# Performance work log

Hardware: AMD Instinct MI355X
Metric: run time of the kernel (lower is better)

The kernel has to match this reference:

```python
import jax, jax.numpy as jnp
import numpy as np

N = 50000      # nodes
E = 640000     # edges
D = 128        # in_dims == hidden_dims == out_dims (heads=1)
PE_DIM = 37
NTYPES = 9     # n_edge_types + 1
L = 3          # n_layers


def setup_inputs() -> dict:
    key = jax.random.key(0)
    ks = jax.random.split(key, 16)
    s = 0.1
    return {
        "X_n": jax.random.normal(ks[0], (N, D), jnp.float32),
        "PE": jax.random.normal(ks[1], (N, PE_DIM), jnp.float32),
        "edge_index": jax.random.randint(ks[2], (2, E), 0, N, jnp.int32),
        "edge_attr": jax.random.randint(ks[3], (E,), 0, NTYPES, jnp.int32),
        # stacked per-layer parameters (all layers share dims since heads=1)
        "edge_emb": jax.random.normal(ks[4], (L, NTYPES, D), jnp.float32) * s,
        "pe_W": jax.random.normal(ks[5], (L, PE_DIM, D), jnp.float32) * s,   # pe MLP modeled as single Linear
        "pe_b": jnp.zeros((L, D), jnp.float32),
        "lin_W": jax.random.normal(ks[6], (L, D, D), jnp.float32) * s,      # [in,out] layout: h @ W
        "attn_l": jax.random.normal(ks[7], (L, D), jnp.float32) * s,
        "attn_r": jax.random.normal(ks[8], (L, D), jnp.float32) * s,
        "attn_e": jax.random.normal(ks[9], (L, D), jnp.float32) * s,
        "bias": jnp.zeros((L, D), jnp.float32),
        "bn_gamma": jnp.ones((L - 1, D), jnp.float32),
        "bn_beta": jnp.zeros((L - 1, D), jnp.float32),
    }


def _gat_forward(X_n, PE, edge_emb, pe_W, pe_b, lin_W, attn_l, attn_r,
                 attn_e, bias, bn_gamma, bn_beta, src, dst, edge_attr):
    x = X_n
    for l in range(L):
        x0 = x
        # PE embedding + linear projection (heads=1 -> per-head dim = D)
        h = x + PE @ pe_W[l] + pe_b[l]
        h = h @ lin_W[l]                                  # [N, D]
        # per-edge attention logits
        xe_score = (edge_emb[l][edge_attr] * attn_e[l]).sum(-1)   # [E]
        hj = h[src]                                       # gather source feats [E, D]
        alpha = hj @ attn_l[l] + (h @ attn_r[l])[dst] + xe_score  # [E]
        alpha = jnp.where(alpha > 0, alpha, 0.2 * alpha)  # leaky_relu(0.2)
        # scatter-softmax over incoming edges of each target node
        amax = jax.ops.segment_max(alpha, dst, num_segments=N)
        e = jnp.exp(alpha - amax[dst])
        denom = jax.ops.segment_sum(e, dst, num_segments=N)
        a = e / denom[dst]                                # [E]
        # weighted scatter-add aggregation
        out = jax.ops.segment_sum(a[:, None] * hj, dst, num_segments=N) + bias[l]
        if l < L - 1:
            # BatchNorm1d in training mode (batch statistics, biased var)
            mu = out.mean(0)
            var = ((out - mu) ** 2).mean(0)
            out = (out - mu) / jnp.sqrt(var + 1e-5) * bn_gamma[l] + bn_beta[l]
        x = out + x0                                      # residual
    return x


def reference(X_n, edge_index, edge_attr, PE, edge_emb, pe_W, pe_b, lin_W,
              attn_l, attn_r, attn_e, bias, bn_gamma, bn_beta):
    src, dst = edge_index[0], edge_index[1]
    return _gat_forward(X_n, PE, edge_emb, pe_W, pe_b, lin_W, attn_l, attn_r,
                        attn_e, bias, bn_gamma, bn_beta, src, dst, edge_attr)
```

## Files before the change

kernel.cpp:

```cpp
#include <hip/hip_runtime.h>
#include <hip/hip_bf16.h>
#include <math.h>

#define NNODES 50000
#define NEDGES 640000
#define DIM    128
#define PEDIM  37
#define KTOT   165
#define KPAD   200
#define PEPAD  64
#define HSTR   136
#define NLAYERS 3
#define NSB    ((NNODES + 255) / 256)
#define NPEB   ((NNODES * 8 + 255) / 256)
#define NGSC   16

using bf16x8 = __attribute__((ext_vector_type(8))) short;
using f32x4  = __attribute__((ext_vector_type(4))) float;

static constexpr size_t alignup(size_t x) { return (x + 255) & ~size_t(255); }
static constexpr size_t OFF_X1   = 0;
static constexpr size_t OFF_X2   = alignup(OFF_X1  + (size_t)NNODES * DIM * 4);
static constexpr size_t OFF_O    = alignup(OFF_X2  + (size_t)NNODES * DIM * 4);
static constexpr size_t OFF_H    = alignup(OFF_O   + (size_t)NNODES * DIM * 4);
static constexpr size_t OFF_PEB  = alignup(OFF_H   + (size_t)NNODES * DIM * 2);
static constexpr size_t OFF_HL   = alignup(OFF_PEB + (size_t)NNODES * PEPAD * 2);
static constexpr size_t OFF_HR   = alignup(OFF_HL  + (size_t)NNODES * 4);
static constexpr size_t OFF_OFFS = alignup(OFF_HR  + (size_t)NNODES * 4);
static constexpr size_t OFF_CUR  = alignup(OFF_OFFS + (size_t)(NNODES + 1) * 4);
static constexpr size_t OFF_CSR  = alignup(OFF_CUR + (size_t)NNODES * 4);
static constexpr size_t OFF_BTG  = alignup(OFF_CSR + (size_t)NEDGES * 4);
static constexpr size_t OFF_B2   = alignup(OFF_BTG + 3 * (size_t)DIM * KPAD * 2);
static constexpr size_t OFF_ET   = alignup(OFF_B2  + 3 * DIM * 4);
static constexpr size_t OFF_GS   = alignup(OFF_ET  + 3 * 16 * 4);
static constexpr size_t OFF_BS   = alignup(OFF_GS  + 2 * NGSC * 256 * 4);
static constexpr size_t OFF_BP   = alignup(OFF_BS  + 256 * 4);
static constexpr size_t WS_NEED  = alignup(OFF_BP  + 256 * 4);

__device__ inline unsigned short f2b(float f) {
    union { float f; unsigned int u; } x; x.f = f;
    unsigned int r = x.u + 0x7FFFu + ((x.u >> 16) & 1u);
    return (unsigned short)(r >> 16);
}
__device__ inline unsigned int pack2(float a, float b) {
    return (unsigned int)f2b(a) | ((unsigned int)f2b(b) << 16);
}

__device__ inline void gload_lds16(const void* g, void* l) {
    __builtin_amdgcn_global_load_lds((const __attribute__((address_space(1))) void*)g,
                                     (__attribute__((address_space(3))) void*)l, 16, 0, 0);
}


__global__ void k_zero_int(int* __restrict__ p, int n) {
    for (int i = blockIdx.x * blockDim.x + threadIdx.x; i < n; i += gridDim.x * blockDim.x)
        p[i] = 0;
}

__global__ void k_count(const int* __restrict__ dstv, int* __restrict__ cnt) {
    for (int e = blockIdx.x * blockDim.x + threadIdx.x; e < NEDGES; e += gridDim.x * blockDim.x)
        atomicAdd(&cnt[dstv[e]], 1);
}

__global__ __launch_bounds__(256) void k_scan1(const int* __restrict__ cnt, int* __restrict__ bsum) {
    __shared__ int ls[256];
    const int i = blockIdx.x * 256 + threadIdx.x;
    ls[threadIdx.x] = (i < NNODES) ? cnt[i] : 0;
    __syncthreads();
    for (int d = 128; d > 0; d >>= 1) {
        if (threadIdx.x < d) ls[threadIdx.x] += ls[threadIdx.x + d];
        __syncthreads();
    }
    if (threadIdx.x == 0) bsum[blockIdx.x] = ls[0];
}

__global__ __launch_bounds__(256) void k_scan2(const int* __restrict__ bsum,
                                               int* __restrict__ bpre, int* __restrict__ offs) {
    __shared__ int ls[256];
    const int t = threadIdx.x;
    ls[t] = (t < NSB) ? bsum[t] : 0;
    __syncthreads();
    for (int d = 1; d < 256; d <<= 1) {
        int v = (t >= d) ? ls[t - d] : 0;
        __syncthreads();
        ls[t] += v;
        __syncthreads();
    }
    bpre[t] = (t == 0) ? 0 : ls[t - 1];
    if (t == 255) offs[NNODES] = ls[255];
}

__global__ __launch_bounds__(256) void k_scan3(const int* __restrict__ cnt,
                                               const int* __restrict__ bpre,
                                               int* __restrict__ offs, int* __restrict__ cur) {
    __shared__ int ls[256];
    const int i = blockIdx.x * 256 + threadIdx.x;
    const int v = (i < NNODES) ? cnt[i] : 0;
    ls[threadIdx.x] = v;
    __syncthreads();
    for (int d = 1; d < 256; d <<= 1) {
        int x = (threadIdx.x >= d) ? ls[threadIdx.x - d] : 0;
        __syncthreads();
        ls[threadIdx.x] += x;
        __syncthreads();
    }
    if (i < NNODES) {
        const int excl = ls[threadIdx.x] - v + bpre[blockIdx.x];
        offs[i] = excl;
        cur[i] = excl;
    }
}

__global__ void k_fill(const int* __restrict__ srcv, const int* __restrict__ dstv,
                       const int* __restrict__ attr, int* __restrict__ cur,
                       int* __restrict__ csr) {
    for (int e = blockIdx.x * blockDim.x + threadIdx.x; e < NEDGES; e += gridDim.x * blockDim.x) {
        int d = dstv[e];
        int pos = atomicAdd(&cur[d], 1);
        csr[pos] = (srcv[e] & 0xFFFF) | (attr[e] << 16);
    }
}

__device__ inline void params_body(int pb, int tid,
    const float* __restrict__ linW, const float* __restrict__ peW,
    const float* __restrict__ peb, const float* __restrict__ attn_e,
    const float* __restrict__ edge_emb,
    unsigned short* __restrict__ Btg, float* __restrict__ b2, float* __restrict__ et) {
    if (pb < 100) {
        const int idx = pb * 256 + tid;
        const int j = idx & 127;
        const int k = idx >> 7;
        float v = 0.f;
        if (k < DIM) {
            v = linW[k * DIM + j];
        } else if (k < KTOT) {
            const int p = k - DIM;
            float s = 0.f;
            #pragma unroll 8
            for (int d = 0; d < DIM; ++d) s = fmaf(peW[p * DIM + d], linW[d * DIM + j], s);
            v = s;
        }
        Btg[(size_t)j * KPAD + k] = f2b(v);
    } else {
        if (tid < DIM) {
            float s = 0.f;
            #pragma unroll 8
            for (int d = 0; d < DIM; ++d) s = fmaf(peb[d], linW[d * DIM + tid], s);
            b2[tid] = s;
        } else if (tid < DIM + 9) {
            const int e = tid - DIM;
            float s = 0.f;
            #pragma unroll 8
            for (int d = 0; d < DIM; ++d) s = fmaf(edge_emb[e * DIM + d], attn_e[d], s);
            et[e] = s;
        }
    }
}

__global__ __launch_bounds__(256) void k_pack(
    const float* __restrict__ PE,
    const float* __restrict__ lin_W, const float* __restrict__ pe_W,
    const float* __restrict__ pe_b, const float* __restrict__ attn_e,
    const float* __restrict__ edge_emb,
    unsigned short* __restrict__ PEb, unsigned short* __restrict__ Btg,
    float* __restrict__ b2, float* __restrict__ et, float* __restrict__ gs) {
    const int b = blockIdx.x;
    if (b < NPEB) {
        const int idx = b * 256 + threadIdx.x;
        if (idx >= NNODES * 8) return;
        const int r = idx >> 3, q = idx & 7;
        float f[8];
        #pragma unroll
        for (int i = 0; i < 8; ++i) {
            const int ci = q * 8 + i;
            f[i] = (ci < PEDIM) ? PE[(size_t)r * PEDIM + ci] : 0.f;
        }
        int4 pk;
        pk.x = pack2(f[0], f[1]); pk.y = pack2(f[2], f[3]);
        pk.z = pack2(f[4], f[5]); pk.w = pack2(f[6], f[7]);
        ((int4*)(PEb + (size_t)r * PEPAD))[q] = pk;
    } else if (b < NPEB + 3 * 101) {
        const int pidx = b - NPEB;
        const int l = pidx / 101, pb = pidx % 101;
        params_body(pb, threadIdx.x,
                    lin_W + (size_t)l * DIM * DIM, pe_W + (size_t)l * PEDIM * DIM,
                    pe_b + (size_t)l * DIM, attn_e + (size_t)l * DIM,
                    edge_emb + (size_t)l * 9 * DIM,
                    Btg + (size_t)l * DIM * KPAD, b2 + l * DIM, et + l * 16);
    } else {
        for (int i = threadIdx.x; i < 2 * NGSC * 256; i += 256) gs[i] = 0.f;
    }
}

template<int L0>
__global__ __launch_bounds__(256) void k_gemm(
    const void* __restrict__ OPREV, const float* __restrict__ XPREV,
    const float* __restrict__ gsrc, const float* __restrict__ gamma,
    const float* __restrict__ beta, float* __restrict__ XNEXT,
    const unsigned short* __restrict__ PEb, const unsigned short* __restrict__ Btg,
    const float* __restrict__ b2, const float* __restrict__ attn_l,
    const float* __restrict__ attn_r,
    unsigned short* __restrict__ H, float* __restrict__ HL, float* __restrict__ HR) {
    __shared__ unsigned short Bls[DIM * KPAD];
    __shared__ float smu[DIM], ssc[DIM], sbt[DIM];
    const int tid = threadIdx.x;
    const int row0 = blockIdx.x * 64;
    const int w = tid >> 6, l = tid & 63;
    const int c = l & 15;
    const int g = l >> 4;
    const int row = row0 + w * 16 + c;
    const bool ok = row < NNODES;

    float4 oxf[4][2], xpv[4][2];
    int4 oxb[4];
    #pragma unroll
    for (int s = 0; s < 4; ++s) {
        const int col0 = g * 8 + s * 32;
        const float4 z = {0.f, 0.f, 0.f, 0.f};
        xpv[s][0] = z; xpv[s][1] = z;
        if (L0) {
            oxf[s][0] = z; oxf[s][1] = z;
            if (ok) {
                const float4* op = (const float4*)&((const float*)OPREV)[((size_t)row << 7) + col0];
                oxf[s][0] = op[0]; oxf[s][1] = op[1];
            }
        } else {
            oxb[s] = make_int4(0, 0, 0, 0);
            if (ok) {
                oxb[s] = *(const int4*)&((const unsigned short*)OPREV)[((size_t)row << 7) + col0];
                const float4* xp = (const float4*)&XPREV[((size_t)row << 7) + col0];
                xpv[s][0] = xp[0]; xpv[s][1] = xp[1];
            }
        }
    }
    int4 pe4 = {0, 0, 0, 0}, pe5 = {0, 0, 0, 0};
    if (ok) {
        const int4* pp = (const int4*)(PEb + (size_t)row * PEPAD);
        pe4 = pp[g];
        pe5 = pp[4 + g];
    }

    {
        const int4* gb = (const int4*)Btg;
        int4* lb = (int4*)Bls;
        for (int i = tid; i < 3200; i += 256) gload_lds16(gb + i, lb + i);
    }
    if (!L0 && tid < DIM) {
        float s = 0.f, s2 = 0.f;
        #pragma unroll
        for (int q = 0; q < NGSC; ++q) {
            s += gsrc[q * 256 + tid];
            s2 += gsrc[q * 256 + 128 + tid];
        }
        const float mu = s * (1.f / NNODES);
        const float var = s2 * (1.f / NNODES) - mu * mu;
        smu[tid] = mu;
        ssc[tid] = gamma[tid] * rsqrtf(var + 1e-5f);
        sbt[tid] = beta[tid];
    }
    __syncthreads();

    bf16x8 af[6];
    #pragma unroll
    for (int s = 0; s < 4; ++s) {
        const int col0 = g * 8 + s * 32;
        float xn[8];
        if (L0) {
            xn[0] = oxf[s][0].x; xn[1] = oxf[s][0].y; xn[2] = oxf[s][0].z; xn[3] = oxf[s][0].w;
            xn[4] = oxf[s][1].x; xn[5] = oxf[s][1].y; xn[6] = oxf[s][1].z; xn[7] = oxf[s][1].w;
        } else {
            const unsigned int u0 = (unsigned)oxb[s].x, u1 = (unsigned)oxb[s].y;
            const unsigned int u2 = (unsigned)oxb[s].z, u3 = (unsigned)oxb[s].w;
            float ov[8];
            ov[0] = __uint_as_float(u0 << 16); ov[1] = __uint_as_float(u0 & 0xFFFF0000u);
            ov[2] = __uint_as_float(u1 << 16); ov[3] = __uint_as_float(u1 & 0xFFFF0000u);
            ov[4] = __uint_as_float(u2 << 16); ov[5] = __uint_as_float(u2 & 0xFFFF0000u);
            ov[6] = __uint_as_float(u3 << 16); ov[7] = __uint_as_float(u3 & 0xFFFF0000u);
            const float4 mu0 = *(const float4*)&smu[col0], mu1 = *(const float4*)&smu[col0 + 4];
            const float4 sc0 = *(const float4*)&ssc[col0], sc1 = *(const float4*)&ssc[col0 + 4];
            const float4 bt0 = *(const float4*)&sbt[col0], bt1 = *(const float4*)&sbt[col0 + 4];
            xn[0] = (ov[0] - mu0.x) * sc0.x + bt0.x + xpv[s][0].x;
            xn[1] = (ov[1] - mu0.y) * sc0.y + bt0.y + xpv[s][0].y;
            xn[2] = (ov[2] - mu0.z) * sc0.z + bt0.z + xpv[s][0].z;
            xn[3] = (ov[3] - mu0.w) * sc0.w + bt0.w + xpv[s][0].w;
            xn[4] = (ov[4] - mu1.x) * sc1.x + bt1.x + xpv[s][1].x;
            xn[5] = (ov[5] - mu1.y) * sc1.y + bt1.y + xpv[s][1].y;
            xn[6] = (ov[6] - mu1.z) * sc1.z + bt1.z + xpv[s][1].z;
            xn[7] = (ov[7] - mu1.w) * sc1.w + bt1.w + xpv[s][1].w;
            if (ok) {
                float4* xo = (float4*)&XNEXT[((size_t)row << 7) + col0];
                xo[0] = make_float4(xn[0], xn[1], xn[2], xn[3]);
                xo[1] = make_float4(xn[4], xn[5], xn[6], xn[7]);
            }
        }
        int4 pk;
        pk.x = pack2(xn[0], xn[1]); pk.y = pack2(xn[2], xn[3]);
        pk.z = pack2(xn[4], xn[5]); pk.w = pack2(xn[6], xn[7]);
        af[s] = *(const bf16x8*)&pk;
    }
    af[4] = *(const bf16x8*)&pe4;
    af[5] = *(const bf16x8*)&pe5;

    f32x4 zero4 = {0.f, 0.f, 0.f, 0.f};
    f32x4 acc[8];
    #pragma unroll
    for (int t = 0; t < 8; ++t) acc[t] = zero4;

    #pragma unroll
    for (int t = 0; t < 8; ++t) {
        const unsigned short* bRow = Bls + (size_t)(t * 16 + c) * KPAD + g * 8;
        #pragma unroll
        for (int s = 0; s < 6; ++s)
            acc[t] = __builtin_amdgcn_mfma_f32_16x16x32_bf16(af[s], *(const bf16x8*)(bRow + s * 32), acc[t], 0, 0, 0);
    }

    float b2v[8], alv[8], arv[8];
    #pragma unroll
    for (int t = 0; t < 8; ++t) {
        b2v[t] = b2[t * 16 + c];
        alv[t] = attn_l[t * 16 + c];
        arv[t] = attn_r[t * 16 + c];
    }
    #pragma unroll
    for (int t = 0; t < 8; ++t)
        #pragma unroll
        for (int j = 0; j < 4; ++j) acc[t][j] += b2v[t];

    #pragma unroll
    for (int j = 0; j < 4; ++j) {
        float sl = 0.f, sr = 0.f;
        #pragma unroll
        for (int t = 0; t < 8; ++t) { sl = fmaf(acc[t][j], alv[t], sl); sr = fmaf(acc[t][j], arv[t], sr); }
        #pragma unroll
        for (int m = 1; m < 16; m <<= 1) {
            sl += __shfl_xor(sl, m, 64);
            sr += __shfl_xor(sr, m, 64);
        }
        const int grow = row0 + w * 16 + g * 4 + j;
        if (grow < NNODES && c == 0) { HL[grow] = sl; HR[grow] = sr; }
    }

    __syncthreads();
    unsigned short* Hls = Bls;
    #pragma unroll
    for (int t = 0; t < 8; ++t)
        #pragma unroll
        for (int j = 0; j < 4; ++j)
            Hls[(w * 16 + g * 4 + j) * HSTR + t * 16 + c] = f2b(acc[t][j]);
    __syncthreads();
    #pragma unroll
    for (int kb = 0; kb < 4; ++kb) {
        const int idx = tid + kb * 256;
        const int r = idx >> 4, kc = idx & 15;
        const int grow = row0 + r;
        if (grow < NNODES) {
            const int4 v = *(const int4*)(Hls + r * HSTR + kc * 8);
            ((int4*)(H + ((size_t)grow << 7)))[kc] = v;
        }
    }
}

template<int FINAL>
__global__ __launch_bounds__(256) void k_agg(
    const int* __restrict__ offs, const int* __restrict__ csr,
    const float* __restrict__ HL, const float* __restrict__ HR,
    const float* __restrict__ et, const unsigned short* __restrict__ H,
    const float* __restrict__ bias, const float* __restrict__ xprev,
    void* __restrict__ OUTv) {
    const int lane = threadIdx.x & 63;
    const int node = blockIdx.x * 4 + (threadIdx.x >> 6);
    const int off0 = offs[node];
    const int deg = offs[node + 1] - off0;

    const float hri = HR[node];
    float myA = 0.f;
    int myE = 0;
    float mx = -1e30f;
    for (int j = lane; j < deg; j += 64) {
        const int en = csr[off0 + j];
        float al = HL[en & 0xFFFF] + hri + et[en >> 16];
        al = al > 0.f ? al : 0.2f * al;
        if (j < 64) { myA = al; myE = en & 0xFFFF; }
        mx = fmaxf(mx, al);
    }
    #pragma unroll
    for (int m = 1; m < 64; m <<= 1) mx = fmaxf(mx, __shfl_xor(mx, m, 64));

    float s = 0.f, wv = 0.f;
    const bool small = deg <= 64;
    if (small) {
        wv = (lane < deg) ? __expf(myA - mx) : 0.f;
        s = wv;
    } else {
        for (int j = lane; j < deg; j += 64) {
            const int en = csr[off0 + j];
            float al = HL[en & 0xFFFF] + hri + et[en >> 16];
            al = al > 0.f ? al : 0.2f * al;
            s += __expf(al - mx);
        }
    }
    #pragma unroll
    for (int m = 1; m < 64; m <<= 1) s += __shfl_xor(s, m, 64);
    const float invd = (deg > 0) ? 1.f / s : 0.f;
    wv *= invd;

    const int eg = lane >> 4, c = lane & 15;
    float a[8];
    #pragma unroll
    for (int t = 0; t < 8; ++t) a[t] = 0.f;

    if (small) {
        for (int jb = 0; jb < deg; jb += 16) {
            float wl[4];
            int sl[4];
            #pragma unroll
            for (int u = 0; u < 4; ++u) {
                const int j = jb + eg + u * 4;
                wl[u] = __shfl(wv, j & 63, 64);
                sl[u] = __shfl(myE, j & 63, 64);
                if (j >= deg) wl[u] = 0.f;
            }
            int4 hv0 = *(const int4*)(H + ((size_t)sl[0] << 7) + (c << 3));
            int4 hv1 = *(const int4*)(H + ((size_t)sl[1] << 7) + (c << 3));
            int4 hv2 = *(const int4*)(H + ((size_t)sl[2] << 7) + (c << 3));
            int4 hv3 = *(const int4*)(H + ((size_t)sl[3] << 7) + (c << 3));
            const int4 hvv[4] = {hv0, hv1, hv2, hv3};
            #pragma unroll
            for (int u = 0; u < 4; ++u) {
                const unsigned int ux = (unsigned)hvv[u].x, uy = (unsigned)hvv[u].y;
                const unsigned int uz = (unsigned)hvv[u].z, uw = (unsigned)hvv[u].w;
                const float wg = wl[u];
                a[0] = fmaf(wg, __uint_as_float(ux << 16), a[0]);
                a[1] = fmaf(wg, __uint_as_float(ux & 0xFFFF0000u), a[1]);
                a[2] = fmaf(wg, __uint_as_float(uy << 16), a[2]);
                a[3] = fmaf(wg, __uint_as_float(uy & 0xFFFF0000u), a[3]);
                a[4] = fmaf(wg, __uint_as_float(uz << 16), a[4]);
                a[5] = fmaf(wg, __uint_as_float(uz & 0xFFFF0000u), a[5]);
                a[6] = fmaf(wg, __uint_as_float(uw << 16), a[6]);
                a[7] = fmaf(wg, __uint_as_float(uw & 0xFFFF0000u), a[7]);
            }
        }
    } else {
        for (int jb = 0; jb < deg; jb += 8) {
            float wl[2];
            int sl[2];
            #pragma unroll
            for (int u = 0; u < 2; ++u) {
                const int j = jb + eg + u * 4;
                wl[u] = 0.f; sl[u] = 0;
                if (j < deg) {
                    const int en = csr[off0 + j];
                    sl[u] = en & 0xFFFF;
                    float al = HL[sl[u]] + hri + et[en >> 16];
                    al = al > 0.f ? al : 0.2f * al;
                    wl[u] = __expf(al - mx) * invd;
                }
            }
            int4 hv0 = *(const int4*)(H + ((size_t)sl[0] << 7) + (c << 3));
            int4 hv1 = *(const int4*)(H + ((size_t)sl[1] << 7) + (c << 3));
            const int4 hvv[2] = {hv0, hv1};
            #pragma unroll
            for (int u = 0; u < 2; ++u) {
                const unsigned int ux = (unsigned)hvv[u].x, uy = (unsigned)hvv[u].y;
                const unsigned int uz = (unsigned)hvv[u].z, uw = (unsigned)hvv[u].w;
                const float wg = wl[u];
                a[0] = fmaf(wg, __uint_as_float(ux << 16), a[0]);
                a[1] = fmaf(wg, __uint_as_float(ux & 0xFFFF0000u), a[1]);
                a[2] = fmaf(wg, __uint_as_float(uy << 16), a[2]);
                a[3] = fmaf(wg, __uint_as_float(uy & 0xFFFF0000u), a[3]);
                a[4] = fmaf(wg, __uint_as_float(uz << 16), a[4]);
                a[5] = fmaf(wg, __uint_as_float(uz & 0xFFFF0000u), a[5]);
                a[6] = fmaf(wg, __uint_as_float(uw << 16), a[6]);
                a[7] = fmaf(wg, __uint_as_float(uw & 0xFFFF0000u), a[7]);
            }
        }
    }

    #pragma unroll
    for (int m = 16; m < 64; m <<= 1)
        #pragma unroll
        for (int t = 0; t < 8; ++t) a[t] += __shfl_xor(a[t], m, 64);

    if (eg == 0) {
        float o[8];
        const float* bp = bias + (c << 3);
        #pragma unroll
        for (int t = 0; t < 8; ++t) o[t] = a[t] + bp[t];
        if (FINAL) {
            float* OUT = (float*)OUTv;
            const float* xp = xprev + ((size_t)node << 7) + (c << 3);
            #pragma unroll
            for (int t = 0; t < 8; ++t) o[t] += xp[t];
            float* op = OUT + ((size_t)node << 7) + (c << 3);
            *(float4*)(op)     = make_float4(o[0], o[1], o[2], o[3]);
            *(float4*)(op + 4) = make_float4(o[4], o[5], o[6], o[7]);
        } else {
            unsigned short* OUT = (unsigned short*)OUTv;
            int4 pk;
            pk.x = pack2(o[0], o[1]); pk.y = pack2(o[2], o[3]);
            pk.z = pack2(o[4], o[5]); pk.w = pack2(o[6], o[7]);
            *(int4*)(OUT + ((size_t)node << 7) + (c << 3)) = pk;
        }
    }
}

__global__ __launch_bounds__(256) void k_bnstats(
    const unsigned short* __restrict__ OUT, float* __restrict__ gs) {
    __shared__ float lsl[256], lsh[256], l2l[256], l2h[256];
    const int c2 = threadIdx.x & 63;
    const int q  = threadIdx.x >> 6;
    const int rend = min(NNODES, (int)(blockIdx.x * 256 + 256));
    const unsigned int* U = (const unsigned int*)OUT;
    float sl = 0.f, sh = 0.f, s2l = 0.f, s2h = 0.f;
    for (int r = blockIdx.x * 256 + q; r < rend; r += 4) {
        const unsigned int u = U[(size_t)r * 64 + c2];
        const float lo = __uint_as_float(u << 16);
        const float hi = __uint_as_float(u & 0xFFFF0000u);
        sl += lo; sh += hi;
        s2l = fmaf(lo, lo, s2l); s2h = fmaf(hi, hi, s2h);
    }
    lsl[threadIdx.x] = sl; lsh[threadIdx.x] = sh;
    l2l[threadIdx.x] = s2l; l2h[threadIdx.x] = s2h;
    __syncthreads();
    if (threadIdx.x < 64) {
        float a0 = 0.f, a1 = 0.f, a2 = 0.f, a3 = 0.f;
        #pragma unroll
        for (int k = 0; k < 4; ++k) {
            a0 += lsl[k * 64 + c2]; a1 += lsh[k * 64 + c2];
            a2 += l2l[k * 64 + c2]; a3 += l2h[k * 64 + c2];
        }
        const int qq = blockIdx.x & (NGSC - 1);
        atomicAdd(&gs[qq * 256 + 2 * c2], a0);
        atomicAdd(&gs[qq * 256 + 2 * c2 + 1], a1);
        atomicAdd(&gs[qq * 256 + 128 + 2 * c2], a2);
        atomicAdd(&gs[qq * 256 + 128 + 2 * c2 + 1], a3);
    }
}

extern "C" void kernel_launch(void* const* d_in, const int* in_sizes, int n_in,
                              void* d_out, int out_size, void* d_ws, size_t ws_size,
                              hipStream_t stream) {
    const float* X_n      = (const float*)d_in[0];
    const float* PE       = (const float*)d_in[1];
    const int*   eidx     = (const int*)d_in[2];
    const int*   eattr    = (const int*)d_in[3];
    const float* edge_emb = (const float*)d_in[4];
    const float* pe_W     = (const float*)d_in[5];
    const float* pe_b     = (const float*)d_in[6];
    const float* lin_W    = (const float*)d_in[7];
    const float* attn_l   = (const float*)d_in[8];
    const float* attn_r   = (const float*)d_in[9];
    const float* attn_e   = (const float*)d_in[10];
    const float* bias     = (const float*)d_in[11];
    const float* bng      = (const float*)d_in[12];
    const float* bnb      = (const float*)d_in[13];

    if (ws_size < WS_NEED) return;

    char* ws = (char*)d_ws;
    float* x1     = (float*)(ws + OFF_X1);
    float* x2     = (float*)(ws + OFF_X2);
    unsigned short* obufb = (unsigned short*)(ws + OFF_O);
    unsigned short* hbuf  = (unsigned short*)(ws + OFF_H);
    unsigned short* PEb   = (unsigned short*)(ws + OFF_PEB);
    float* hl     = (float*)(ws + OFF_HL);
    float* hr     = (float*)(ws + OFF_HR);
    int*   offs   = (int*)(ws + OFF_OFFS);
    int*   cur    = (int*)(ws + OFF_CUR);
    int*   csr    = (int*)(ws + OFF_CSR);
    unsigned short* Btg = (unsigned short*)(ws + OFF_BTG);
    float* b2     = (float*)(ws + OFF_B2);
    float* et     = (float*)(ws + OFF_ET);
    float* gs     = (float*)(ws + OFF_GS);
    int*   bsum   = (int*)(ws + OFF_BS);
    int*   bpre   = (int*)(ws + OFF_BP);

    const int* srcv = eidx;
    const int* dstv = eidx + NEDGES;

    hipLaunchKernelGGL(k_zero_int, dim3(256), dim3(256), 0, stream, cur, NNODES);
    hipLaunchKernelGGL(k_count, dim3(1024), dim3(256), 0, stream, dstv, cur);
    hipLaunchKernelGGL(k_scan1, dim3(NSB), dim3(256), 0, stream, cur, bsum);
    hipLaunchKernelGGL(k_scan2, dim3(1), dim3(256), 0, stream, bsum, bpre, offs);
    hipLaunchKernelGGL(k_scan3, dim3(NSB), dim3(256), 0, stream, cur, bpre, offs, cur);
    hipLaunchKernelGGL(k_fill, dim3(1024), dim3(256), 0, stream, srcv, dstv, eattr, cur, csr);
    hipLaunchKernelGGL(k_pack, dim3(NPEB + 3 * 101 + 1), dim3(256), 0, stream,
                       PE, lin_W, pe_W, pe_b, attn_e, edge_emb, PEb, Btg, b2, et, gs);

    const int NGB = (NNODES + 63) / 64;
    hipLaunchKernelGGL((k_gemm<1>), dim3(NGB), dim3(256), 0, stream,
                       (const void*)X_n, (const float*)nullptr, (const float*)nullptr,
                       (const float*)nullptr, (const float*)nullptr, (float*)nullptr,
                       PEb, Btg, b2, attn_l, attn_r, hbuf, hl, hr);
    hipLaunchKernelGGL((k_agg<0>), dim3(NNODES / 4), dim3(256), 0, stream,
                       offs, csr, hl, hr, et, hbuf, bias, (const float*)nullptr, (void*)obufb);
    hipLaunchKernelGGL(k_bnstats, dim3(NSB), dim3(256), 0, stream, obufb, gs);
    hipLaunchKernelGGL((k_gemm<0>), dim3(NGB), dim3(256), 0, stream,
                       (const void*)obufb, X_n, gs, bng, bnb, x1,
                       PEb, Btg + (size_t)DIM * KPAD, b2 + DIM, attn_l + DIM, attn_r + DIM,
                       hbuf, hl, hr);
    hipLaunchKernelGGL((k_agg<0>), dim3(NNODES / 4), dim3(256), 0, stream,
                       offs, csr, hl, hr, et + 16, hbuf, bias + DIM, (const float*)nullptr, (void*)obufb);
    hipLaunchKernelGGL(k_bnstats, dim3(NSB), dim3(256), 0, stream, obufb, gs + NGSC * 256);
    hipLaunchKernelGGL((k_gemm<0>), dim3(NGB), dim3(256), 0, stream,
                       (const void*)obufb, x1, gs + NGSC * 256, bng + DIM, bnb + DIM, x2,
                       PEb, Btg + 2 * (size_t)DIM * KPAD, b2 + 2 * DIM, attn_l + 2 * DIM, attn_r + 2 * DIM,
                       hbuf, hl, hr);
    hipLaunchKernelGGL((k_agg<1>), dim3(NNODES / 4), dim3(256), 0, stream,
                       offs, csr, hl, hr, et + 32, hbuf, bias + 2 * DIM, x2,
                       (void*)d_out);
}
```

Before: 275.5 us.

## Bucket CSR fill in two passes and store residual activations as bf16

The CSR build now runs in two passes. Edges are first scattered into 32-node buckets using one atomic counter per bucket, padded to 64 bytes. A second per-bucket kernel then sorts each bucket by node in LDS and writes the result with coalesced stores. This is meant to cut global atomic contention and scattered writes, at the cost of an extra kernel and a temp buffer. Separately, the intermediate residual states x1/x2 are stored as bf16 instead of fp32, which halves their read/write traffic but adds rounding error to the residual path.

```diff
diff --git a/kernel.cpp b/kernel.cpp
--- a/kernel.cpp
+++ b/kernel.cpp
@@ -14,22 +14,26 @@
 #define NSB    ((NNODES + 255) / 256)
 #define NPEB   ((NNODES * 8 + 255) / 256)
 #define NGSC   16
+#define NBUCK  ((NNODES + 31) / 32)
+#define FCAP   1280
 
 using bf16x8 = __attribute__((ext_vector_type(8))) short;
 using f32x4  = __attribute__((ext_vector_type(4))) float;
 
 static constexpr size_t alignup(size_t x) { return (x + 255) & ~size_t(255); }
 static constexpr size_t OFF_X1   = 0;
-static constexpr size_t OFF_X2   = alignup(OFF_X1  + (size_t)NNODES * DIM * 4);
-static constexpr size_t OFF_O    = alignup(OFF_X2  + (size_t)NNODES * DIM * 4);
-static constexpr size_t OFF_H    = alignup(OFF_O   + (size_t)NNODES * DIM * 4);
+static constexpr size_t OFF_X2   = alignup(OFF_X1  + (size_t)NNODES * DIM * 2);
+static constexpr size_t OFF_O    = alignup(OFF_X2  + (size_t)NNODES * DIM * 2);
+static constexpr size_t OFF_H    = alignup(OFF_O   + (size_t)NNODES * DIM * 2);
 static constexpr size_t OFF_PEB  = alignup(OFF_H   + (size_t)NNODES * DIM * 2);
 static constexpr size_t OFF_HL   = alignup(OFF_PEB + (size_t)NNODES * PEPAD * 2);
 static constexpr size_t OFF_HR   = alignup(OFF_HL  + (size_t)NNODES * 4);
 static constexpr size_t OFF_OFFS = alignup(OFF_HR  + (size_t)NNODES * 4);
 static constexpr size_t OFF_CUR  = alignup(OFF_OFFS + (size_t)(NNODES + 1) * 4);
 static constexpr size_t OFF_CSR  = alignup(OFF_CUR + (size_t)NNODES * 4);
-static constexpr size_t OFF_BTG  = alignup(OFF_CSR + (size_t)NEDGES * 4);
+static constexpr size_t OFF_TMP  = alignup(OFF_CSR + (size_t)NEDGES * 4);
+static constexpr size_t OFF_BCUR = alignup(OFF_TMP + (size_t)NEDGES * 4);
+static constexpr size_t OFF_BTG  = alignup(OFF_BCUR + (size_t)NBUCK * 64);
 static constexpr size_t OFF_B2   = alignup(OFF_BTG + 3 * (size_t)DIM * KPAD * 2);
 static constexpr size_t OFF_ET   = alignup(OFF_B2  + 3 * DIM * 4);
 static constexpr size_t OFF_GS   = alignup(OFF_ET  + 3 * 16 * 4);
@@ -92,7 +96,8 @@
 
 __global__ __launch_bounds__(256) void k_scan3(const int* __restrict__ cnt,
                                                const int* __restrict__ bpre,
-                                               int* __restrict__ offs, int* __restrict__ cur) {
+                                               int* __restrict__ offs, int* __restrict__ cur,
+                                               int* __restrict__ bcur) {
     __shared__ int ls[256];
     const int i = blockIdx.x * 256 + threadIdx.x;
     const int v = (i < NNODES) ? cnt[i] : 0;
@@ -108,16 +113,52 @@
         const int excl = ls[threadIdx.x] - v + bpre[blockIdx.x];
         offs[i] = excl;
         cur[i] = excl;
-    }
-}
-
-__global__ void k_fill(const int* __restrict__ srcv, const int* __restrict__ dstv,
-                       const int* __restrict__ attr, int* __restrict__ cur,
-                       int* __restrict__ csr) {
+        if ((i & 31) == 0) bcur[(i >> 5) * 16] = excl;
+    }
+}
+
+__global__ void k_fillA(const int* __restrict__ srcv, const int* __restrict__ dstv,
+                        const int* __restrict__ attr, int* __restrict__ bcur,
+                        int* __restrict__ tmp) {
     for (int e = blockIdx.x * blockDim.x + threadIdx.x; e < NEDGES; e += gridDim.x * blockDim.x) {
-        int d = dstv[e];
-        int pos = atomicAdd(&cur[d], 1);
-        csr[pos] = (srcv[e] & 0xFFFF) | (attr[e] << 16);
+        const int d = dstv[e];
+        const int pos = atomicAdd(&bcur[(d >> 5) * 16], 1);
+        tmp[pos] = (srcv[e] & 0xFFFF) | (attr[e] << 16) | ((d & 31) << 20);
+    }
+}
+
+__global__ __launch_bounds__(256) void k_fillB(const int* __restrict__ offs,
+                                               const int* __restrict__ tmp,
+                                               int* __restrict__ cur, int* __restrict__ csr) {
+    __shared__ int cur32[32];
+    __shared__ int sdata[FCAP];
+    const int b = blockIdx.x;
+    const int nb = b * 32;
+    const int nbe = min(nb + 32, NNODES);
+    const int start = offs[nb];
+    const int end = offs[nbe];
+    const int size = end - start;
+    if (threadIdx.x < 32) {
+        const int node = nb + threadIdx.x;
+        cur32[threadIdx.x] = ((node < nbe) ? offs[node] : end) - start;
+    }
+    __syncthreads();
+    if (size <= FCAP) {
+        for (int i = threadIdx.x; i < size; i += 256) {
+            const int v = tmp[start + i];
+            const int p = atomicAdd(&cur32[(v >> 20) & 31], 1);
+            sdata[p] = v & 0xFFFFF;
+        }
+        __syncthreads();
+        for (int i = threadIdx.x; i < size; i += 256)
+            csr[start + i] = sdata[i];
+    } else {
+        for (int i = threadIdx.x; i < size; i += 256) {
+            const int v = tmp[start + i];
+            const int node = nb + ((v >> 20) & 31);
+            const int p = atomicAdd(&cur[node], 1);
+            csr[p] = v & 0xFFFFF;
+        }
     }
 }
 
@@ -192,11 +233,11 @@
     }
 }
 
-template<int L0>
+template<int MODE>
 __global__ __launch_bounds__(256) void k_gemm(
-    const void* __restrict__ OPREV, const float* __restrict__ XPREV,
+    const void* __restrict__ OPREV, const void* __restrict__ XPREV,
     const float* __restrict__ gsrc, const float* __restrict__ gamma,
-    const float* __restrict__ beta, float* __restrict__ XNEXT,
+    const float* __restrict__ beta, unsigned short* __restrict__ XNEXT,
     const unsigned short* __restrict__ PEb, const unsigned short* __restrict__ Btg,
     const float* __restrict__ b2, const float* __restrict__ attn_l,
     const float* __restrict__ attn_r,
@@ -211,14 +252,13 @@
     const int row = row0 + w * 16 + c;
     const bool ok = row < NNODES;
 
-    float4 oxf[4][2], xpv[4][2];
-    int4 oxb[4];
+    float4 oxf[4][2], xpf[4][2];
+    int4 oxb[4], xpb[4];
     #pragma unroll
     for (int s = 0; s < 4; ++s) {
         const int col0 = g * 8 + s * 32;
         const float4 z = {0.f, 0.f, 0.f, 0.f};
-        xpv[s][0] = z; xpv[s][1] = z;
-        if (L0) {
+        if (MODE == 0) {
             oxf[s][0] = z; oxf[s][1] = z;
             if (ok) {
                 const float4* op = (const float4*)&((const float*)OPREV)[((size_t)row << 7) + col0];
@@ -226,10 +266,16 @@
             }
         } else {
             oxb[s] = make_int4(0, 0, 0, 0);
-            if (ok) {
-                oxb[s] = *(const int4*)&((const unsigned short*)OPREV)[((size_t)row << 7) + col0];
-                const float4* xp = (const float4*)&XPREV[((size_t)row << 7) + col0];
-                xpv[s][0] = xp[0]; xpv[s][1] = xp[1];
+            if (ok) oxb[s] = *(const int4*)&((const unsigned short*)OPREV)[((size_t)row << 7) + col0];
+            if (MODE == 1) {
+                xpf[s][0] = z; xpf[s][1] = z;
+                if (ok) {
+                    const float4* xp = (const float4*)&((const float*)XPREV)[((size_t)row << 7) + col0];
+                    xpf[s][0] = xp[0]; xpf[s][1] = xp[1];
+                }
+            } else {
+                xpb[s] = make_int4(0, 0, 0, 0);
+                if (ok) xpb[s] = *(const int4*)&((const unsigned short*)XPREV)[((size_t)row << 7) + col0];
             }
         }
     }
@@ -245,7 +291,7 @@
         int4* lb = (int4*)Bls;
         for (int i = tid; i < 3200; i += 256) gload_lds16(gb + i, lb + i);
     }
-    if (!L0 && tid < DIM) {
+    if (MODE != 0 && tid < DIM) {
         float s = 0.f, s2 = 0.f;
         #pragma unroll
         for (int q = 0; q < NGSC; ++q) {
@@ -265,7 +311,7 @@
     for (int s = 0; s < 4; ++s) {
         const int col0 = g * 8 + s * 32;
         float xn[8];
-        if (L0) {
+        if (MODE == 0) {
             xn[0] = oxf[s][0].x; xn[1] = oxf[s][0].y; xn[2] = oxf[s][0].z; xn[3] = oxf[s][0].w;
             xn[4] = oxf[s][1].x; xn[5] = oxf[s][1].y; xn[6] = oxf[s][1].z; xn[7] = oxf[s][1].w;
         } else {
@@ -276,26 +322,35 @@
             ov[2] = __uint_as_float(u1 << 16); ov[3] = __uint_as_float(u1 & 0xFFFF0000u);
             ov[4] = __uint_as_float(u2 << 16); ov[5] = __uint_as_float(u2 & 0xFFFF0000u);
             ov[6] = __uint_as_float(u3 << 16); ov[7] = __uint_as_float(u3 & 0xFFFF0000u);
+            float xv[8];
+            if (MODE == 1) {
+                xv[0] = xpf[s][0].x; xv[1] = xpf[s][0].y; xv[2] = xpf[s][0].z; xv[3] = xpf[s][0].w;
+                xv[4] = xpf[s][1].x; xv[5] = xpf[s][1].y; xv[6] = xpf[s][1].z; xv[7] = xpf[s][1].w;
+            } else {
+                const unsigned int p0 = (unsigned)xpb[s].x, p1 = (unsigned)xpb[s].y;
+                const unsigned int p2 = (unsigned)xpb[s].z, p3 = (unsigned)xpb[s].w;
+                xv[0] = __uint_as_float(p0 << 16); xv[1] = __uint_as_float(p0 & 0xFFFF0000u);
+                xv[2] = __uint_as_float(p1 << 16); xv[3] = __uint_as_float(p1 & 0xFFFF0000u);
+                xv[4] = __uint_as_float(p2 << 16); xv[5] = __uint_as_float(p2 & 0xFFFF0000u);
+                xv[6] = __uint_as_float(p3 << 16); xv[7] = __uint_as_float(p3 & 0xFFFF0000u);
+            }
             const float4 mu0 = *(const float4*)&smu[col0], mu1 = *(const float4*)&smu[col0 + 4];
             const float4 sc0 = *(const float4*)&ssc[col0], sc1 = *(const float4*)&ssc[col0 + 4];
             const float4 bt0 = *(const float4*)&sbt[col0], bt1 = *(const float4*)&sbt[col0 + 4];
-            xn[0] = (ov[0] - mu0.x) * sc0.x + bt0.x + xpv[s][0].x;
-            xn[1] = (ov[1] - mu0.y) * sc0.y + bt0.y + xpv[s][0].y;
-            xn[2] = (ov[2] - mu0.z) * sc0.z + bt0.z + xpv[s][0].z;
-            xn[3] = (ov[3] - mu0.w) * sc0.w + bt0.w + xpv[s][0].w;
-            xn[4] = (ov[4] - mu1.x) * sc1.x + bt1.x + xpv[s][1].x;
-            xn[5] = (ov[5] - mu1.y) * sc1.y + bt1.y + xpv[s][1].y;
-            xn[6] = (ov[6] - mu1.z) * sc1.z + bt1.z + xpv[s][1].z;
-            xn[7] = (ov[7] - mu1.w) * sc1.w + bt1.w + xpv[s][1].w;
-            if (ok) {
-                float4* xo = (float4*)&XNEXT[((size_t)row << 7) + col0];
-                xo[0] = make_float4(xn[0], xn[1], xn[2], xn[3]);
-                xo[1] = make_float4(xn[4], xn[5], xn[6], xn[7]);
-            }
+            xn[0] = (ov[0] - mu0.x) * sc0.x + bt0.x + xv[0];
+            xn[1] = (ov[1] - mu0.y) * sc0.y + bt0.y + xv[1];
+            xn[2] = (ov[2] - mu0.z) * sc0.z + bt0.z + xv[2];
+            xn[3] = (ov[3] - mu0.w) * sc0.w + bt0.w + xv[3];
+            xn[4] = (ov[4] - mu1.x) * sc1.x + bt1.x + xv[4];
+            xn[5] = (ov[5] - mu1.y) * sc1.y + bt1.y + xv[5];
+            xn[6] = (ov[6] - mu1.z) * sc1.z + bt1.z + xv[6];
+            xn[7] = (ov[7] - mu1.w) * sc1.w + bt1.w + xv[7];
         }
         int4 pk;
         pk.x = pack2(xn[0], xn[1]); pk.y = pack2(xn[2], xn[3]);
         pk.z = pack2(xn[4], xn[5]); pk.w = pack2(xn[6], xn[7]);
+        if (MODE != 0 && ok)
+            *(int4*)&XNEXT[((size_t)row << 7) + col0] = pk;
         af[s] = *(const bf16x8*)&pk;
     }
     af[4] = *(const bf16x8*)&pe4;
@@ -365,7 +420,7 @@
     const int* __restrict__ offs, const int* __restrict__ csr,
     const float* __restrict__ HL, const float* __restrict__ HR,
     const float* __restrict__ et, const unsigned short* __restrict__ H,
-    const float* __restrict__ bias, const float* __restrict__ xprev,
+    const float* __restrict__ bias, const unsigned short* __restrict__ xprev,
     void* __restrict__ OUTv) {
     const int lane = threadIdx.x & 63;
     const int node = blockIdx.x * 4 + (threadIdx.x >> 6);
@@ -488,9 +543,13 @@
         for (int t = 0; t < 8; ++t) o[t] = a[t] + bp[t];
         if (FINAL) {
             float* OUT = (float*)OUTv;
-            const float* xp = xprev + ((size_t)node << 7) + (c << 3);
-            #pragma unroll
-            for (int t = 0; t < 8; ++t) o[t] += xp[t];
+            const int4 xb = *(const int4*)(xprev + ((size_t)node << 7) + (c << 3));
+            const unsigned int p0 = (unsigned)xb.x, p1 = (unsigned)xb.y;
+            const unsigned int p2 = (unsigned)xb.z, p3 = (unsigned)xb.w;
+            o[0] += __uint_as_float(p0 << 16); o[1] += __uint_as_float(p0 & 0xFFFF0000u);
+            o[2] += __uint_as_float(p1 << 16); o[3] += __uint_as_float(p1 & 0xFFFF0000u);
+            o[4] += __uint_as_float(p2 << 16); o[5] += __uint_as_float(p2 & 0xFFFF0000u);
+            o[6] += __uint_as_float(p3 << 16); o[7] += __uint_as_float(p3 & 0xFFFF0000u);
             float* op = OUT + ((size_t)node << 7) + (c << 3);
             *(float4*)(op)     = make_float4(o[0], o[1], o[2], o[3]);
             *(float4*)(op + 4) = make_float4(o[4], o[5], o[6], o[7]);
@@ -558,8 +617,8 @@
     if (ws_size < WS_NEED) return;
 
     char* ws = (char*)d_ws;
-    float* x1     = (float*)(ws + OFF_X1);
-    float* x2     = (float*)(ws + OFF_X2);
+    unsigned short* x1    = (unsigned short*)(ws + OFF_X1);
+    unsigned short* x2    = (unsigned short*)(ws + OFF_X2);
     unsigned short* obufb = (unsigned short*)(ws + OFF_O);
     unsigned short* hbuf  = (unsigned short*)(ws + OFF_H);
     unsigned short* PEb   = (unsigned short*)(ws + OFF_PEB);
@@ -568,6 +627,8 @@
     int*   offs   = (int*)(ws + OFF_OFFS);
     int*   cur    = (int*)(ws + OFF_CUR);
     int*   csr    = (int*)(ws + OFF_CSR);
+    int*   tmp    = (int*)(ws + OFF_TMP);
+    int*   bcur   = (int*)(ws + OFF_BCUR);
     unsigned short* Btg = (unsigned short*)(ws + OFF_BTG);
     float* b2     = (float*)(ws + OFF_B2);
     float* et     = (float*)(ws + OFF_ET);
@@ -582,28 +643,29 @@
     hipLaunchKernelGGL(k_count, dim3(1024), dim3(256), 0, stream, dstv, cur);
     hipLaunchKernelGGL(k_scan1, dim3(NSB), dim3(256), 0, stream, cur, bsum);
     hipLaunchKernelGGL(k_scan2, dim3(1), dim3(256), 0, stream, bsum, bpre, offs);
-    hipLaunchKernelGGL(k_scan3, dim3(NSB), dim3(256), 0, stream, cur, bpre, offs, cur);
-    hipLaunchKernelGGL(k_fill, dim3(1024), dim3(256), 0, stream, srcv, dstv, eattr, cur, csr);
+    hipLaunchKernelGGL(k_scan3, dim3(NSB), dim3(256), 0, stream, cur, bpre, offs, cur, bcur);
+    hipLaunchKernelGGL(k_fillA, dim3(1024), dim3(256), 0, stream, srcv, dstv, eattr, bcur, tmp);
+    hipLaunchKernelGGL(k_fillB, dim3(NBUCK), dim3(256), 0, stream, offs, tmp, cur, csr);
     hipLaunchKernelGGL(k_pack, dim3(NPEB + 3 * 101 + 1), dim3(256), 0, stream,
                        PE, lin_W, pe_W, pe_b, attn_e, edge_emb, PEb, Btg, b2, et, gs);
 
     const int NGB = (NNODES + 63) / 64;
-    hipLaunchKernelGGL((k_gemm<1>), dim3(NGB), dim3(256), 0, stream,
-                       (const void*)X_n, (const float*)nullptr, (const float*)nullptr,
-                       (const float*)nullptr, (const float*)nullptr, (float*)nullptr,
+    hipLaunchKernelGGL((k_gemm<0>), dim3(NGB), dim3(256), 0, stream,
+                       (const void*)X_n, (const void*)nullptr, (const float*)nullptr,
+                       (const float*)nullptr, (const float*)nullptr, (unsigned short*)nullptr,
                        PEb, Btg, b2, attn_l, attn_r, hbuf, hl, hr);
     hipLaunchKernelGGL((k_agg<0>), dim3(NNODES / 4), dim3(256), 0, stream,
-                       offs, csr, hl, hr, et, hbuf, bias, (const float*)nullptr, (void*)obufb);
+                       offs, csr, hl, hr, et, hbuf, bias, (const unsigned short*)nullptr, (void*)obufb);
     hipLaunchKernelGGL(k_bnstats, dim3(NSB), dim3(256), 0, stream, obufb, gs);
-    hipLaunchKernelGGL((k_gemm<0>), dim3(NGB), dim3(256), 0, stream,
-                       (const void*)obufb, X_n, gs, bng, bnb, x1,
+    hipLaunchKernelGGL((k_gemm<1>), dim3(NGB), dim3(256), 0, stream,
+                       (const void*)obufb, (const void*)X_n, gs, bng, bnb, x1,
                        PEb, Btg + (size_t)DIM * KPAD, b2 + DIM, attn_l + DIM, attn_r + DIM,
                        hbuf, hl, hr);
     hipLaunchKernelGGL((k_agg<0>), dim3(NNODES / 4), dim3(256), 0, stream,
-                       offs, csr, hl, hr, et + 16, hbuf, bias + DIM, (const float*)nullptr, (void*)obufb);
+                       offs, csr, hl, hr, et + 16, hbuf, bias + DIM, (const unsigned short*)nullptr, (void*)obufb);
     hipLaunchKernelGGL(k_bnstats, dim3(NSB), dim3(256), 0, stream, obufb, gs + NGSC * 256);
-    hipLaunchKernelGGL((k_gemm<0>), dim3(NGB), dim3(256), 0, stream,
-                       (const void*)obufb, x1, gs + NGSC * 256, bng + DIM, bnb + DIM, x2,
+    hipLaunchKernelGGL((k_gemm<2>), dim3(NGB), dim3(256), 0, stream,
+                       (const void*)obufb, (const void*)x1, gs + NGSC * 256, bng + DIM, bnb + DIM, x2,
                        PEb, Btg + 2 * (size_t)DIM * KPAD, b2 + 2 * DIM, attn_l + 2 * DIM, attn_r + 2 * DIM,
                        hbuf, hl, hr);
     hipLaunchKernelGGL((k_agg<1>), dim3(NNODES / 4), dim3(256), 0, stream,
```

After: 272.7 us. Within noise of the previous version (-1.0%).
